# Kernel tuning notes

Hardware: AMD Instinct MI355X
Metric: run time of the kernel (lower is better)

## Reference

```python
import jax, jax.numpy as jnp
import numpy as np

H = 16        # num_heads
E = 1024      # embed_size
OUT = 1024    # out_dim
TEMP = 1.0
EPS = 1e-20
LN_EPS = 1e-5


def setup_inputs() -> dict:
    key = jax.random.key(0)
    ks = jax.random.split(key, 16)
    B, S = 8, 4096
    s = 1.0 / np.sqrt(E)
    inp = {
        'x': jax.random.normal(ks[0], (B, S, E), dtype=jnp.float32),
        'gumbel_u': jax.random.uniform(ks[1], (B, H, S, 2), dtype=jnp.float32, minval=1e-6, maxval=1.0 - 1e-6),
        'query': jax.random.uniform(ks[2], (1, E), dtype=jnp.float32, minval=-s, maxval=s),  # xavier-ish
        'Wq': jax.random.uniform(ks[3], (E, E), jnp.float32, -s, s),
        'bq': jnp.zeros((E,), jnp.float32),
        'Wk': jax.random.uniform(ks[4], (E, E), jnp.float32, -s, s),
        'bk': jnp.zeros((E,), jnp.float32),
        'Wv': jax.random.uniform(ks[5], (E, E), jnp.float32, -s, s),
        'bv': jnp.zeros((E,), jnp.float32),
        'ln_g': jnp.ones((E,), jnp.float32),
        'ln_b': jnp.zeros((E,), jnp.float32),
        'W1': jax.random.uniform(ks[6], (4 * E, E), jnp.float32, -s, s),
        'b1': jnp.zeros((4 * E,), jnp.float32),
        'W2': jax.random.uniform(ks[7], (OUT, 4 * E), jnp.float32, -0.5 * s, 0.5 * s),
        'b2': jnp.zeros((OUT,), jnp.float32),
    }
    return inp


def reference(x, gumbel_u, query, Wq, bq, Wk, bk, Wv, bv, ln_g, ln_b, W1, b1, W2, b2):
    B, S, _ = x.shape
    dk = E // H
    # projections
    q = (query @ Wq.T + bq).reshape(H, dk)                      # [H, dk] (single query, broadcast over batch)
    k = (x @ Wk.T + bk).reshape(B, S, H, dk)                    # [B, S, H, dk]
    v = (x @ Wv.T + bv).reshape(B, S, H, dk)
    # single-query attention logits
    logits = jnp.einsum('hd,bshd->bhs', q, k) / np.sqrt(dk)     # [B, H, S]
    probs = jax.nn.softmax(logits, axis=-1)                     # [B, H, S]
    # gumbel-softmax hard mask over {keep=0-logit, drop/keep pair}
    edges = jnp.stack([jnp.zeros_like(logits), logits], axis=-1)  # [B, H, S, 2]
    g = -jnp.log(-jnp.log(gumbel_u + EPS) + EPS)
    y_soft = jax.nn.softmax((edges + g) / TEMP, axis=-1)
    idx = jnp.argmax(y_soft, axis=-1)
    y_hard = jax.nn.one_hot(idx, 2, dtype=y_soft.dtype)
    y = jax.lax.stop_gradient(y_hard - y_soft) + y_soft         # straight-through
    A = y[..., 1]                                               # [B, H, S]
    probs = A * probs
    # weighted sum of values; merge heads (seq_len of query is 1)
    hidden = jnp.einsum('bhs,bshd->bhd', probs, v).reshape(B, E)
    # layernorm
    mu = hidden.mean(axis=-1, keepdims=True)
    var = hidden.var(axis=-1, keepdims=True)
    hidden = (hidden - mu) / jnp.sqrt(var + LN_EPS) * ln_g + ln_b
    # MLP (dropout p=0 -> identity)
    out = jax.nn.relu(hidden @ W1.T + b1) @ W2.T + b2           # [B, OUT]
    masks = A.sum(axis=1)[:, None, :]                           # sum_heads=True -> [B, 1, S]
    attn = probs.sum(axis=1)[:, None, :]
    return out, masks, attn
```

## Files before the change

kernel.cpp:

```cpp
#include <hip/hip_runtime.h>
#include <hip/hip_bf16.h>
#include <math.h>

#define SS 4096
#define EE 1024
#define HH 16

typedef __bf16 bf16x8 __attribute__((ext_vector_type(8)));
typedef float  f32x4v __attribute__((ext_vector_type(4)));

#define OFF_QVEC 0L
#define OFF_QKB  1024L
#define OFF_QH   1040L
#define OFF_QL   9232L
#define OFF_SEC  17424L
#define OFF_SAC  50192L
#define OFF_WG   82960L
#define OFF_HID  607248L
#define OFF_T1   615440L
#define OFF_PX   648208L
#define OFF_GTH  4842512L

__device__ __forceinline__ float bf2f(unsigned int u){
  union { unsigned int i; float f; } c; c.i = u << 16; return c.f;
}
__device__ __forceinline__ unsigned int pk_hi(float a, float b){
  return __builtin_amdgcn_perm(__float_as_uint(b), __float_as_uint(a), 0x07060302u);
}
__device__ __forceinline__ float lo_part(float f){
  return f - __uint_as_float(__float_as_uint(f) & 0xFFFF0000u);
}
__device__ __forceinline__ unsigned short f2bf_rn(float f){
  unsigned int u = __float_as_uint(f);
  return (unsigned short)((u + 0x7fffu + ((u >> 16) & 1u)) >> 16);
}
__device__ __forceinline__ f32x4v mfma16(bf16x8 a, bf16x8 b, f32x4v c){
  return __builtin_amdgcn_mfma_f32_16x16x32_bf16(a, b, c, 0, 0, 0);
}
__device__ __forceinline__ float waveRedSum(float v){
  #pragma unroll
  for (int m=1;m<64;m<<=1) v += __shfl_xor(v, m, 64);
  return v;
}
template<int NW>
__device__ __forceinline__ float blockRedSum(float v, volatile float* scr){
  v = waveRedSum(v);
  const int w = threadIdx.x >> 6;
  __syncthreads();
  if ((threadIdx.x & 63) == 0) scr[w] = v;
  __syncthreads();
  float r = 0.f;
  #pragma unroll
  for (int i=0;i<NW;i++) r += scr[i];
  return r;
}
__device__ __forceinline__ double gdiff(float u0, float u1){
  const double g0 = -log(-log((double)u0 + 1e-20) + 1e-20);
  const double g1 = -log(-log((double)u1 + 1e-20) + 1e-20);
  return g0 - g1;
}

__global__ __launch_bounds__(256) void k1(const float* __restrict__ query, const float* __restrict__ Wq,
                                          const float* __restrict__ bq, const float* __restrict__ gum,
                                          const float* __restrict__ b2,
                                          float* __restrict__ qvec, double* __restrict__ gth,
                                          float* __restrict__ hid, float* __restrict__ out){
  const int t = threadIdx.x;
  const int wv = t >> 6, lane = t & 63;
  const int bid = blockIdx.x;
  if (bid < 256){
    const int j = bid*4 + wv;
    float p = 0.f;
    #pragma unroll
    for (int i=0;i<4;i++){
      const int e = 4*lane + 256*i;
      const float4 q4 = *(const float4*)(query + e);
      const float4 w4 = *(const float4*)(Wq + (long)j*EE + e);
      p += q4.x*w4.x + q4.y*w4.y + q4.z*w4.z + q4.w*w4.w;
    }
    p = waveRedSum(p);
    if (lane == 0) qvec[j] = p + bq[j];
  } else {
    const int ib = bid - 256;
    if (ib < 32) hid[ib*256 + t] = 0.f;
    else if (ib < 64) out[(ib-32)*256 + t] = b2[((ib-32)&3)*256 + t];
    const long i0 = (long)ib*1024 + t*4;
    const float4 a4 = *(const float4*)(gum + 2*i0);
    const float4 b4 = *(const float4*)(gum + 2*i0 + 4);
    gth[i0+0] = gdiff(a4.x, a4.y);
    gth[i0+1] = gdiff(a4.z, a4.w);
    gth[i0+2] = gdiff(b4.x, b4.y);
    gth[i0+3] = gdiff(b4.z, b4.w);
  }
}

__global__ __launch_bounds__(256) void k2(const float* __restrict__ Wk, const float* __restrict__ bk,
                                          const float* __restrict__ qvec,
                                          unsigned short* __restrict__ qh, unsigned short* __restrict__ ql,
                                          float* __restrict__ qkb){
  __shared__ float red[4][64];
  const int wv = threadIdx.x >> 6, lane = threadIdx.x & 63;
  const int h = blockIdx.y;
  const int e = blockIdx.x*64 + lane;
  float acc = 0.f;
  #pragma unroll
  for (int dd=0; dd<16; dd++){
    const int d = wv*16 + dd;
    acc += qvec[h*64+d] * Wk[(long)(h*64+d)*EE + e];
  }
  red[wv][lane] = acc;
  __syncthreads();
  if (wv == 0){
    const float s = red[0][lane] + red[1][lane] + red[2][lane] + red[3][lane];
    const unsigned int ub = __float_as_uint(s);
    qh[h*EE + e] = (unsigned short)(ub >> 16);
    const float lo = s - __uint_as_float(ub & 0xFFFF0000u);
    ql[h*EE + e] = (unsigned short)(__float_as_uint(lo) >> 16);
    if (blockIdx.x == 0){
      float p = qvec[h*64+lane] * bk[h*64+lane];
      p = waveRedSum(p);
      if (lane == 0) qkb[h] = p;
    }
  }
}

__global__ __launch_bounds__(256,2) void k3f(const float* __restrict__ x, const double* __restrict__ gth,
                                             const unsigned short* __restrict__ qh, const unsigned short* __restrict__ ql,
                                             const float* __restrict__ qkb,
                                             float* __restrict__ seC, float* __restrict__ saC,
                                             float* __restrict__ Wg, unsigned short* __restrict__ px,
                                             float* __restrict__ out){
  __shared__ unsigned int xsT[4][256*16];
  __shared__ float lg[4*16*17];
  __shared__ float wT[16][20];
  __shared__ float scrA[16*17], scrB[16*17];
  __shared__ float sQkb[16];
  const int t = threadIdx.x;
  const int wv = t >> 6, lane = t & 63;
  const int m16 = lane & 15, q = lane >> 4;
  const int blk = blockIdx.x, b = blockIdx.y;
  if (t < 16) sQkb[t] = qkb[t];
  unsigned int* xw32 = &xsT[wv][0];
  const unsigned short* xw16 = (const unsigned short*)xw32;

  f32x4v P[16];
  #pragma unroll
  for (int i=0;i<16;i++){ P[i][0]=0.f; P[i][1]=0.f; P[i][2]=0.f; P[i][3]=0.f; }

  for (int ch=0; ch<4; ch++){
    const int c = blk*4 + ch;
    const long xbase = ((long)(b*SS + c*16))*EE;

    f32x4v a = {0.f,0.f,0.f,0.f};
    #pragma unroll
    for (int kt=0; kt<8; kt++){
      const int k = wv*256 + kt*32 + q*8;
      const float* xp = x + xbase + (long)m16*EE + k;
      const float4 f0 = *(const float4*)(xp);
      const float4 f1 = *(const float4*)(xp + 4);
      union { uint4 u; bf16x8 v; } xh, xl, bh, bl;
      xh.u.x = pk_hi(f0.x, f0.y); xh.u.y = pk_hi(f0.z, f0.w);
      xh.u.z = pk_hi(f1.x, f1.y); xh.u.w = pk_hi(f1.z, f1.w);
      xl.u.x = pk_hi(lo_part(f0.x), lo_part(f0.y)); xl.u.y = pk_hi(lo_part(f0.z), lo_part(f0.w));
      xl.u.z = pk_hi(lo_part(f1.x), lo_part(f1.y)); xl.u.w = pk_hi(lo_part(f1.z), lo_part(f1.w));
      bh.u = *(const uint4*)(qh + (long)m16*EE + k);
      bl.u = *(const uint4*)(ql + (long)m16*EE + k);
      a = mfma16(xh.v, bh.v, a);
      a = mfma16(xh.v, bl.v, a);
      a = mfma16(xl.v, bh.v, a);
      const unsigned hw[4] = {xh.u.x, xh.u.y, xh.u.z, xh.u.w};
      const unsigned lw[4] = {xl.u.x, xl.u.y, xl.u.z, xl.u.w};
      const int rowbase = (kt*32 + q*8)*16 + m16;
      #pragma unroll
      for (int jj=0; jj<8; jj++){
        const unsigned val = __builtin_amdgcn_perm(lw[jj>>1], hw[jj>>1],
                                                   (jj & 1) ? 0x07060302u : 0x05040100u);
        xw32[rowbase + jj*16] = val;
      }
    }
    #pragma unroll
    for (int r=0;r<4;r++)
      lg[(wv*16 + q*4 + r)*17 + m16] = a[r];
    __syncthreads();

    {
      const int h = t & 15, s = t >> 4;
      const float dot = lg[s*17+h] + lg[(16+s)*17+h] + lg[(32+s)*17+h] + lg[(48+s)*17+h];
      const float logit = (dot + sQkb[h]) * 0.125f;
      const long gi = ((long)(b*16 + h))*SS + c*16 + s;
      const double gthd = gth[gi];
      const float e = expf(logit);
      const float wval = ((double)logit > gthd) ? e : 0.f;
      wT[h][s] = wval;
      Wg[((long)b*SS + c*16 + s)*16 + h] = wval;
      scrA[s*17 + h] = e;
      scrB[s*17 + h] = wval;
    }
    __syncthreads();

    if (t < 16){
      float S = 0.f, SA = 0.f, cnt = 0.f;
      #pragma unroll
      for (int i=0;i<16;i++){ S += scrA[i*17 + t]; SA += scrB[i*17 + t]; }
      #pragma unroll
      for (int hh=0; hh<16; hh++) cnt += (scrB[t*17 + hh] > 0.f) ? 1.f : 0.f;
      seC[((long)(b*16 + t))*256 + c] = S;
      saC[((long)(b*16 + t))*256 + c] = SA;
      out[8192 + (long)b*SS + c*16 + t] = cnt;
    }

    {
      const float4 w4 = *(const float4*)&wT[m16][q*4];
      union { uint4 u; bf16x8 v; } B1, B2;
      B1.u.x = pk_hi(w4.x, w4.x); B1.u.y = pk_hi(w4.y, w4.y);
      B1.u.z = pk_hi(w4.z, w4.z); B1.u.w = pk_hi(w4.w, w4.w);
      const float l0 = lo_part(w4.x), l1 = lo_part(w4.y), l2 = lo_part(w4.z), l3 = lo_part(w4.w);
      B2.u.x = pk_hi(l0, l0); B2.u.y = pk_hi(l1, l1);
      B2.u.z = pk_hi(l2, l2); B2.u.w = pk_hi(l3, l3);
      #pragma unroll
      for (int et=0; et<16; et++){
        union { uint4 u; bf16x8 v; } A;
        A.u = *(const uint4*)(xw16 + (et*16 + m16)*32 + q*8);
        P[et] = mfma16(A.v, B1.v, P[et]);
        P[et] = mfma16(A.v, B2.v, P[et]);
      }
    }
  }

  const long pbase = (((long)(b*64 + blk))*16 + m16)*1024 + wv*256;
  #pragma unroll
  for (int et=0; et<16; et++){
    uint2 pk2;
    pk2.x = (unsigned)f2bf_rn(P[et][0]) | ((unsigned)f2bf_rn(P[et][1]) << 16);
    pk2.y = (unsigned)f2bf_rn(P[et][2]) | ((unsigned)f2bf_rn(P[et][3]) << 16);
    *(uint2*)(px + pbase + et*16 + q*4) = pk2;
  }
}

__global__ __launch_bounds__(256) void kb(const unsigned short* __restrict__ px, const float* __restrict__ Wg,
                                          const float* __restrict__ seC, const float* __restrict__ saC,
                                          const float* __restrict__ Wv, const float* __restrict__ bv,
                                          float* __restrict__ hid, float* __restrict__ out){
  __shared__ float s_red[16][17];
  __shared__ float sInv[16];
  __shared__ float scr1[4], scr2[4];
  __shared__ float xs[256];
  const int t = threadIdx.x;

  if (blockIdx.x < 32){
    const int b = blockIdx.x >> 2, sq = blockIdx.x & 3;
    { const int h = t >> 4, cl = t & 15;
      float se = 0.f;
      #pragma unroll
      for (int k=0;k<16;k++) se += seC[((long)(b*16+h))*256 + cl + 16*k];
      s_red[h][cl] = se;
    }
    __syncthreads();
    if (t < 16){
      float D = 0.f;
      #pragma unroll
      for (int i=0;i<16;i++) D += s_red[t][i];
      sInv[t] = 1.f / D;
    }
    __syncthreads();
    #pragma unroll
    for (int it=0; it<4; it++){
      const int s = sq*1024 + it*256 + t;
      const float* wr = Wg + ((long)b*SS + s)*16;
      float a = 0.f;
      #pragma unroll
      for (int h=0;h<16;h++) a += wr[h]*sInv[h];
      out[40960 + (long)b*SS + s] = a;
    }
    return;
  }

  const int idx = blockIdx.x - 32;
  const int b = idx >> 6, h = (idx >> 2) & 15, eq = idx & 3;
  const long rbase = ((long)(b*16 + h))*256;
  const float D    = blockRedSum<4>(seC[rbase + t], scr1);
  const float SA   = blockRedSum<4>(saC[rbase + t], scr2);
  const float invD = 1.f / D;
  const float psum = SA * invD;
  const unsigned short* pp = px + (((long)(b*64))*16 + h)*1024 + eq*256 + t;
  float xa = 0.f;
  #pragma unroll 8
  for (int seg=0; seg<64; seg++) xa += bf2f((unsigned)pp[(long)seg*16384]);
  xs[t] = xa;
  __syncthreads();
  const int wv = t >> 6, lane = t & 63;
  const float4 xv = *(const float4*)(xs + 4*lane);
  #pragma unroll 4
  for (int jj=0; jj<16; jj++){
    const int j = h*64 + wv*16 + jj;
    const float4 w4 = *(const float4*)(Wv + (long)j*EE + eq*256 + 4*lane);
    float pr = xv.x*w4.x + xv.y*w4.y + xv.z*w4.z + xv.w*w4.w;
    pr = waveRedSum(pr);
    if (lane == 0){
      float add = pr * invD;
      if (eq == 0) add += psum * bv[j];
      atomicAdd(&hid[(long)b*EE + j], add);
    }
  }
}

__global__ __launch_bounds__(256) void k8f(const float* __restrict__ hid, const float* __restrict__ lng,
                                           const float* __restrict__ lnb, const float* __restrict__ W1,
                                           const float* __restrict__ b1,
                                           unsigned short* __restrict__ t1u){
  __shared__ unsigned short h2[16*1032];
  __shared__ float red[4*64*4];
  const int t = threadIdx.x;
  {
    const int r = t >> 5, ll = t & 31;
    float4 vv[8];
    float s1 = 0.f, s2 = 0.f;
    #pragma unroll
    for (int i=0;i<8;i++){
      vv[i] = *(const float4*)(hid + (long)r*1024 + ll*32 + i*4);
      s1 += vv[i].x + vv[i].y + vv[i].z + vv[i].w;
      s2 += vv[i].x*vv[i].x + vv[i].y*vv[i].y + vv[i].z*vv[i].z + vv[i].w*vv[i].w;
    }
    #pragma unroll
    for (int m=1;m<32;m<<=1){ s1 += __shfl_xor(s1, m, 32); s2 += __shfl_xor(s2, m, 32); }
    const float mu  = s1 * (1.f/1024.f);
    const float var = s2 * (1.f/1024.f) - mu*mu;
    const float rs  = rsqrtf(var + 1e-5f);
    #pragma unroll
    for (int i=0;i<8;i++){
      const int e = ll*32 + i*4;
      const float4 g4 = *(const float4*)(lng + e);
      const float4 b4 = *(const float4*)(lnb + e);
      uint2 pk;
      pk.x = (unsigned)f2bf_rn((vv[i].x-mu)*rs*g4.x + b4.x) | ((unsigned)f2bf_rn((vv[i].y-mu)*rs*g4.y + b4.y) << 16);
      pk.y = (unsigned)f2bf_rn((vv[i].z-mu)*rs*g4.z + b4.z) | ((unsigned)f2bf_rn((vv[i].w-mu)*rs*g4.w + b4.w) << 16);
      *(uint2*)(h2 + r*1032 + e) = pk;
      *(uint2*)(h2 + (8+r)*1032 + e) = make_uint2(0u, 0u);
    }
  }
  __syncthreads();
  const int wv = t >> 6, lane = t & 63;
  const int m16 = lane & 15, q = lane >> 4;
  const int j = blockIdx.x*16 + m16;
  f32x4v a = {0.f,0.f,0.f,0.f};
  #pragma unroll
  for (int kt=0; kt<8; kt++){
    const int k = wv*256 + kt*32 + q*8;
    union { uint4 u; bf16x8 v; } A, B;
    A.u = *(const uint4*)(h2 + m16*1032 + k);
    const float4 f0 = *(const float4*)(W1 + (long)j*EE + k);
    const float4 f1 = *(const float4*)(W1 + (long)j*EE + k + 4);
    B.u.x = pk_hi(f0.x,f0.y); B.u.y = pk_hi(f0.z,f0.w);
    B.u.z = pk_hi(f1.x,f1.y); B.u.w = pk_hi(f1.z,f1.w);
    a = mfma16(A.v, B.v, a);
  }
  #pragma unroll
  for (int r=0;r<4;r++) red[(wv*64 + lane)*4 + r] = a[r];
  __syncthreads();
  if (wv == 0){
    #pragma unroll
    for (int r=0;r<4;r++){
      const float s = red[lane*4+r] + red[(64+lane)*4+r] + red[(128+lane)*4+r] + red[(192+lane)*4+r];
      const int row = q*4 + r;
      const float val = (row < 8) ? fmaxf(s + b1[j], 0.f) : 0.f;
      t1u[(long)row*4096 + j] = f2bf_rn(val);
    }
  }
}

__global__ __launch_bounds__(256) void k9a(const unsigned short* __restrict__ t1u, const float* __restrict__ W2,
                                           float* __restrict__ out){
  __shared__ float red[4*64*4];
  const int wv = threadIdx.x >> 6, lane = threadIdx.x & 63;
  const int m16 = lane & 15, q = lane >> 4;
  const int o = blockIdx.x*16 + m16;
  const int kbase = blockIdx.y*1024 + wv*256;
  f32x4v a = {0.f,0.f,0.f,0.f};
  #pragma unroll
  for (int kt=0; kt<8; kt++){
    const int k = kbase + kt*32 + q*8;
    union { uint4 u; bf16x8 v; } A, B;
    A.u = *(const uint4*)(t1u + (long)m16*4096 + k);
    const float4 f0 = *(const float4*)(W2 + (long)o*4096 + k);
    const float4 f1 = *(const float4*)(W2 + (long)o*4096 + k + 4);
    B.u.x = pk_hi(f0.x,f0.y); B.u.y = pk_hi(f0.z,f0.w);
    B.u.z = pk_hi(f1.x,f1.y); B.u.w = pk_hi(f1.z,f1.w);
    a = mfma16(A.v, B.v, a);
  }
  #pragma unroll
  for (int r=0;r<4;r++) red[(wv*64 + lane)*4 + r] = a[r];
  __syncthreads();
  if (wv == 0){
    #pragma unroll
    for (int r=0;r<4;r++){
      const int row = q*4 + r;
      if (row < 8){
        const float s = red[lane*4+r] + red[(64+lane)*4+r] + red[(128+lane)*4+r] + red[(192+lane)*4+r];
        atomicAdd(out + row*1024 + o, s);
      }
    }
  }
}

extern "C" void kernel_launch(void* const* d_in, const int* in_sizes, int n_in,
                              void* d_out, int out_size, void* d_ws, size_t ws_size,
                              hipStream_t stream){
  const float* x    = (const float*)d_in[0];
  const float* gum  = (const float*)d_in[1];
  const float* query= (const float*)d_in[2];
  const float* Wq   = (const float*)d_in[3];
  const float* bq   = (const float*)d_in[4];
  const float* Wk   = (const float*)d_in[5];
  const float* bk   = (const float*)d_in[6];
  const float* Wv   = (const float*)d_in[7];
  const float* bv   = (const float*)d_in[8];
  const float* lng  = (const float*)d_in[9];
  const float* lnb  = (const float*)d_in[10];
  const float* W1   = (const float*)d_in[11];
  const float* b1   = (const float*)d_in[12];
  const float* W2   = (const float*)d_in[13];
  const float* b2   = (const float*)d_in[14];
  float* ws = (float*)d_ws;
  float* qvec = ws + OFF_QVEC;
  float* qkb  = ws + OFF_QKB;
  unsigned short* qh = (unsigned short*)(ws + OFF_QH);
  unsigned short* ql = (unsigned short*)(ws + OFF_QL);
  float* seC  = ws + OFF_SEC;
  float* saC  = ws + OFF_SAC;
  float* Wg   = ws + OFF_WG;
  float* hid  = ws + OFF_HID;
  unsigned short* t1u = (unsigned short*)(ws + OFF_T1);
  unsigned short* px  = (unsigned short*)(ws + OFF_PX);
  double* gth = (double*)(ws + OFF_GTH);
  float* out = (float*)d_out;

  k1  <<<768, 256, 0, stream>>>(query, Wq, bq, gum, b2, qvec, gth, hid, out);
  k2  <<<dim3(16,16), 256, 0, stream>>>(Wk, bk, qvec, qh, ql, qkb);
  k3f <<<dim3(64,8), 256, 0, stream>>>(x, gth, qh, ql, qkb, seC, saC, Wg, px, out);
  kb  <<<544, 256, 0, stream>>>(px, Wg, seC, saC, Wv, bv, hid, out);
  k8f <<<256, 256, 0, stream>>>(hid, lng, lnb, W1, b1, t1u);
  k9a <<<dim3(64,4), 256, 0, stream>>>(t1u, W2, out);
}
```

Baseline: 291.1 us.

## Pad LDS transpose buffer, pack px stores into 16-byte writes, permute reduction layout

```diff
diff --git a/kernel.cpp b/kernel.cpp
--- a/kernel.cpp
+++ b/kernel.cpp
@@ -33,6 +33,9 @@
 __device__ __forceinline__ unsigned short f2bf_rn(float f){
   unsigned int u = __float_as_uint(f);
   return (unsigned short)((u + 0x7fffu + ((u >> 16) & 1u)) >> 16);
+}
+__device__ __forceinline__ unsigned int pk2bf(float a, float b){
+  return (unsigned)f2bf_rn(a) | ((unsigned)f2bf_rn(b) << 16);
 }
 __device__ __forceinline__ f32x4v mfma16(bf16x8 a, bf16x8 b, f32x4v c){
   return __builtin_amdgcn_mfma_f32_16x16x32_bf16(a, b, c, 0, 0, 0);
@@ -130,10 +133,10 @@
                                              float* __restrict__ seC, float* __restrict__ saC,
                                              float* __restrict__ Wg, unsigned short* __restrict__ px,
                                              float* __restrict__ out){
-  __shared__ unsigned int xsT[4][256*16];
-  __shared__ float lg[4*16*17];
-  __shared__ float wT[16][20];
-  __shared__ float scrA[16*17], scrB[16*17];
+  __shared__ unsigned int xsT[4][256*18];
+  __shared__ float lg[4*16*16];
+  __shared__ float wT[16*20];
+  __shared__ float wE[16*20];
   __shared__ float sQkb[16];
   const int t = threadIdx.x;
   const int wv = t >> 6, lane = t & 63;
@@ -141,7 +144,6 @@
   const int blk = blockIdx.x, b = blockIdx.y;
   if (t < 16) sQkb[t] = qkb[t];
   unsigned int* xw32 = &xsT[wv][0];
-  const unsigned short* xw16 = (const unsigned short*)xw32;
 
   f32x4v P[16];
   #pragma unroll
@@ -170,70 +172,76 @@
       a = mfma16(xl.v, bh.v, a);
       const unsigned hw[4] = {xh.u.x, xh.u.y, xh.u.z, xh.u.w};
       const unsigned lw[4] = {xl.u.x, xl.u.y, xl.u.z, xl.u.w};
-      const int rowbase = (kt*32 + q*8)*16 + m16;
+      const int rowbase = (kt*32 + q*8)*18 + m16;
       #pragma unroll
       for (int jj=0; jj<8; jj++){
         const unsigned val = __builtin_amdgcn_perm(lw[jj>>1], hw[jj>>1],
                                                    (jj & 1) ? 0x07060302u : 0x05040100u);
-        xw32[rowbase + jj*16] = val;
+        xw32[rowbase + jj*18] = val;
       }
     }
     #pragma unroll
     for (int r=0;r<4;r++)
-      lg[(wv*16 + q*4 + r)*17 + m16] = a[r];
+      lg[(wv*16 + q*4 + r)*16 + m16] = a[r];
     __syncthreads();
 
     {
       const int h = t & 15, s = t >> 4;
-      const float dot = lg[s*17+h] + lg[(16+s)*17+h] + lg[(32+s)*17+h] + lg[(48+s)*17+h];
+      const float dot = lg[s*16+h] + lg[(16+s)*16+h] + lg[(32+s)*16+h] + lg[(48+s)*16+h];
       const float logit = (dot + sQkb[h]) * 0.125f;
       const long gi = ((long)(b*16 + h))*SS + c*16 + s;
       const double gthd = gth[gi];
       const float e = expf(logit);
       const float wval = ((double)logit > gthd) ? e : 0.f;
-      wT[h][s] = wval;
+      wT[h*20 + s] = wval;
+      wE[h*20 + s] = e;
       Wg[((long)b*SS + c*16 + s)*16 + h] = wval;
-      scrA[s*17 + h] = e;
-      scrB[s*17 + h] = wval;
     }
     __syncthreads();
 
     if (t < 16){
       float S = 0.f, SA = 0.f, cnt = 0.f;
       #pragma unroll
-      for (int i=0;i<16;i++){ S += scrA[i*17 + t]; SA += scrB[i*17 + t]; }
-      #pragma unroll
-      for (int hh=0; hh<16; hh++) cnt += (scrB[t*17 + hh] > 0.f) ? 1.f : 0.f;
+      for (int i=0;i<16;i++){ S += wE[t*20 + i]; SA += wT[t*20 + i]; }
+      #pragma unroll
+      for (int hh=0; hh<16; hh++) cnt += (wT[hh*20 + t] > 0.f) ? 1.f : 0.f;
       seC[((long)(b*16 + t))*256 + c] = S;
       saC[((long)(b*16 + t))*256 + c] = SA;
       out[8192 + (long)b*SS + c*16 + t] = cnt;
     }
 
     {
-      const float4 w4 = *(const float4*)&wT[m16][q*4];
+      float wf[4];
+      *(float4*)&wf[0] = *(const float4*)&wT[m16*20 + q*4];
       union { uint4 u; bf16x8 v; } B1, B2;
-      B1.u.x = pk_hi(w4.x, w4.x); B1.u.y = pk_hi(w4.y, w4.y);
-      B1.u.z = pk_hi(w4.z, w4.z); B1.u.w = pk_hi(w4.w, w4.w);
-      const float l0 = lo_part(w4.x), l1 = lo_part(w4.y), l2 = lo_part(w4.z), l3 = lo_part(w4.w);
+      B1.u.x = pk_hi(wf[0],wf[0]); B1.u.y = pk_hi(wf[1],wf[1]);
+      B1.u.z = pk_hi(wf[2],wf[2]); B1.u.w = pk_hi(wf[3],wf[3]);
+      const float l0 = lo_part(wf[0]), l1 = lo_part(wf[1]), l2 = lo_part(wf[2]), l3 = lo_part(wf[3]);
       B2.u.x = pk_hi(l0, l0); B2.u.y = pk_hi(l1, l1);
       B2.u.z = pk_hi(l2, l2); B2.u.w = pk_hi(l3, l3);
       #pragma unroll
       for (int et=0; et<16; et++){
+        const int rb = (et*16 + m16)*18 + q*4;
         union { uint4 u; bf16x8 v; } A;
-        A.u = *(const uint4*)(xw16 + (et*16 + m16)*32 + q*8);
+        const uint2 a01 = *(const uint2*)(xw32 + rb);
+        const uint2 a23 = *(const uint2*)(xw32 + rb + 2);
+        A.u.x = a01.x; A.u.y = a01.y; A.u.z = a23.x; A.u.w = a23.y;
         P[et] = mfma16(A.v, B1.v, P[et]);
         P[et] = mfma16(A.v, B2.v, P[et]);
       }
     }
   }
 
-  const long pbase = (((long)(b*64 + blk))*16 + m16)*1024 + wv*256;
-  #pragma unroll
-  for (int et=0; et<16; et++){
-    uint2 pk2;
-    pk2.x = (unsigned)f2bf_rn(P[et][0]) | ((unsigned)f2bf_rn(P[et][1]) << 16);
-    pk2.y = (unsigned)f2bf_rn(P[et][2]) | ((unsigned)f2bf_rn(P[et][3]) << 16);
-    *(uint2*)(px + pbase + et*16 + q*4) = pk2;
+  const long pbase = (((long)(b*64 + blk))*16 + m16)*1024 + wv*256 + q*64;
+  #pragma unroll
+  for (int ep=0; ep<8; ep++){
+    const int et = ep*2;
+    uint4 pk4;
+    pk4.x = pk2bf(P[et][0],   P[et][1]);
+    pk4.y = pk2bf(P[et][2],   P[et][3]);
+    pk4.z = pk2bf(P[et+1][0], P[et+1][1]);
+    pk4.w = pk2bf(P[et+1][2], P[et+1][3]);
+    *(uint4*)(px + pbase + et*4) = pk4;
   }
 }
 
@@ -286,7 +294,8 @@
   float xa = 0.f;
   #pragma unroll 8
   for (int seg=0; seg<64; seg++) xa += bf2f((unsigned)pp[(long)seg*16384]);
-  xs[t] = xa;
+  const int eloc = ((t>>2)&15)*16 + ((t>>6)&3)*4 + (t&3);
+  xs[eloc] = xa;
   __syncthreads();
   const int wv = t >> 6, lane = t & 63;
   const float4 xv = *(const float4*)(xs + 4*lane);
@@ -332,8 +341,8 @@
       const float4 g4 = *(const float4*)(lng + e);
       const float4 b4 = *(const float4*)(lnb + e);
       uint2 pk;
-      pk.x = (unsigned)f2bf_rn((vv[i].x-mu)*rs*g4.x + b4.x) | ((unsigned)f2bf_rn((vv[i].y-mu)*rs*g4.y + b4.y) << 16);
-      pk.y = (unsigned)f2bf_rn((vv[i].z-mu)*rs*g4.z + b4.z) | ((unsigned)f2bf_rn((vv[i].w-mu)*rs*g4.w + b4.w) << 16);
+      pk.x = pk2bf((vv[i].x-mu)*rs*g4.x + b4.x, (vv[i].y-mu)*rs*g4.y + b4.y);
+      pk.y = pk2bf((vv[i].z-mu)*rs*g4.z + b4.z, (vv[i].w-mu)*rs*g4.w + b4.w);
       *(uint2*)(h2 + r*1032 + e) = pk;
       *(uint2*)(h2 + (8+r)*1032 + e) = make_uint2(0u, 0u);
     }
```

After: 293.3 us. Within noise of the previous version (+0.7%).
